# Performance work log

Hardware: AMD Instinct MI355X
Metric: run time of the kernel (lower is better)

Reference implementation:

```python
import jax, jax.numpy as jnp
import numpy as np
from jax import lax

H = 1024
VOCAB = 32000
B = 64
T = 256
PAD_IDX = 0


def setup_inputs() -> dict:
    key = jax.random.key(0)
    ks = jax.random.split(key, 10)
    tgt = jax.random.randint(ks[0], (B, T), 0, VOCAB, dtype=jnp.int64)
    h0 = jax.random.normal(ks[1], (1, B, H), dtype=jnp.float32)
    c0 = jax.random.normal(ks[2], (1, B, H), dtype=jnp.float32)
    encoder_outputs = jax.random.normal(ks[3], (B, 64, H), dtype=jnp.float32)
    src_lengths = jax.random.randint(ks[4], (B,), 1, 64, dtype=jnp.int64)
    # Embedding table; padding_idx row is zero (as nn.Embedding with padding_idx)
    scale = 1.0 / np.sqrt(H)
    emb = jax.random.normal(ks[5], (VOCAB, H), dtype=jnp.float32)
    emb = emb.at[PAD_IDX].set(0.0)
    # LSTM params, PyTorch layout: W_ih [4H, H], W_hh [4H, H], gate order i,f,g,o
    W_ih = jax.random.uniform(ks[6], (4 * H, H), minval=-scale, maxval=scale, dtype=jnp.float32)
    W_hh = jax.random.uniform(ks[7], (4 * H, H), minval=-scale, maxval=scale, dtype=jnp.float32)
    b_ih = jax.random.uniform(ks[8], (4 * H,), minval=-scale, maxval=scale, dtype=jnp.float32)
    b_hh = jax.random.uniform(ks[9], (4 * H,), minval=-scale, maxval=scale, dtype=jnp.float32)
    return {"tgt": tgt, "h0": h0, "c0": c0, "encoder_outputs": encoder_outputs,
            "src_lengths": src_lengths, "emb": emb,
            "W_ih": W_ih, "W_hh": W_hh, "b_ih": b_ih, "b_hh": b_hh}


def reference(tgt, h0, c0, encoder_outputs, src_lengths, emb, W_ih, W_hh, b_ih, b_hh):
    # Dropout in eval mode => identity. attn / encoder_outputs / src_lengths unused in math.
    x = emb[tgt]                      # [B, T, H] embedding lookup
    bias = b_ih + b_hh                # [4H]
    # Precompute input projections for all steps at once (same math, one big GEMM)
    x_proj = jnp.einsum('bth,gh->btg', x, W_ih) + bias   # [B, T, 4H]

    def step(carry, xp_t):
        h, c = carry                  # [B, H] each
        gates = xp_t + h @ W_hh.T     # [B, 4H]
        i, f, g, o = jnp.split(gates, 4, axis=-1)
        c_new = jax.nn.sigmoid(f) * c + jax.nn.sigmoid(i) * jnp.tanh(g)
        h_new = jax.nn.sigmoid(o) * jnp.tanh(c_new)
        return (h_new, c_new), h_new

    (h_fin, c_fin), ys = lax.scan(step, (h0[0], c0[0]),
                                  jnp.swapaxes(x_proj, 0, 1))   # scan over T
    outputs = jnp.swapaxes(ys, 0, 1)  # [B, T, H]
    return outputs, (h_fin[None], c_fin[None])
```

## Files before the change

### kernel.cpp

```cpp
#include <hip/hip_runtime.h>
#include <hip/hip_bf16.h>
#include <math.h>

#define B    64
#define T    256
#define H    1024
#define G4   4096
#define TC   64
#define NCH  (T / TC)
#define NBLK 128
#define FSTR 16

typedef __attribute__((ext_vector_type(8))) short bf16x8;
typedef __attribute__((ext_vector_type(4))) float f32x4;

__device__ __forceinline__ unsigned short f2bf(float x) {
    union { float f; unsigned u; } v; v.f = x;
    unsigned r = v.u + 0x7fffu + ((v.u >> 16) & 1u);
    return (unsigned short)(r >> 16);
}
__device__ __forceinline__ float bf2f(unsigned short s) {
    union { unsigned u; float f; } v; v.u = ((unsigned)s) << 16;
    return v.f;
}
__device__ __forceinline__ float sigm_f(float x) {
    return 1.f / (1.f + __expf(-x));
}
__device__ __forceinline__ float tanh_f(float x) {
    float e = __expf(2.f * x);
    return (e - 1.f) / (e + 1.f);
}

__global__ __launch_bounds__(256) void cast_f32_bf16(
    const float* __restrict__ src, unsigned short* __restrict__ dst, int n8)
{
    int i = blockIdx.x * 256 + threadIdx.x;
    if (i >= n8) return;
    const float4* s = (const float4*)(src + (size_t)i * 8);
    float4 a = s[0], b = s[1];
    bf16x8 o;
    o[0] = f2bf(a.x); o[1] = f2bf(a.y); o[2] = f2bf(a.z); o[3] = f2bf(a.w);
    o[4] = f2bf(b.x); o[5] = f2bf(b.y); o[6] = f2bf(b.z); o[7] = f2bf(b.w);
    *(bf16x8*)(dst + (size_t)i * 8) = o;
}

__global__ __launch_bounds__(256) void gather_x(
    const int* __restrict__ tgt, const float* __restrict__ emb,
    unsigned short* __restrict__ xch, int t0)
{
    int tid = threadIdx.x;
    int r   = blockIdx.x * 2 + (tid >> 7);
    int c   = (tid & 127) * 8;
    int b   = r & 63, tcc = r >> 6;
    int token = tgt[b * T + t0 + tcc];
    const float4* s = (const float4*)(emb + (size_t)token * H + c);
    float4 x0 = s[0], x1 = s[1];
    bf16x8 o;
    o[0] = f2bf(x0.x); o[1] = f2bf(x0.y); o[2] = f2bf(x0.z); o[3] = f2bf(x0.w);
    o[4] = f2bf(x1.x); o[5] = f2bf(x1.y); o[6] = f2bf(x1.z); o[7] = f2bf(x1.w);
    *(bf16x8*)(xch + (size_t)r * H + c) = o;
}

__global__ __launch_bounds__(256) void gemm_xproj(
    const unsigned short* __restrict__ A,
    const unsigned short* __restrict__ Bt,
    unsigned short* __restrict__ C)
{
    __shared__ unsigned short As[128 * 64], Bs[128 * 64];
    const int tid  = threadIdx.x;
    const int brow = (blockIdx.x >> 5) * 128;
    const int bcol = (blockIdx.x & 31) * 128;
    const int w = tid >> 6, lane = tid & 63;
    const int wr = w >> 1, wc = w & 1;
    const int lr = lane & 15, lg = lane >> 4;

    f32x4 acc[4][4] = {};

    for (int kc = 0; kc < H; kc += 64) {
        if (kc) __syncthreads();
        #pragma unroll
        for (int i = 0; i < 4; ++i) {
            int sf  = i * 256 + tid;
            int row = sf >> 3, s = sf & 7;
            int col = kc + s * 8;
            *(bf16x8*)(As + row * 64 + ((s ^ (row & 7)) * 8)) =
                *(const bf16x8*)(A + (size_t)(brow + row) * H + col);
            *(bf16x8*)(Bs + row * 64 + ((s ^ (row & 7)) * 8)) =
                *(const bf16x8*)(Bt + (size_t)(bcol + row) * H + col);
        }
        __syncthreads();
        #pragma unroll
        for (int kk = 0; kk < 2; ++kk) {
            bf16x8 af[4], bv[4];
            #pragma unroll
            for (int m = 0; m < 4; ++m) {
                int row = wr * 64 + m * 16 + lr;
                int s   = kk * 4 + lg;
                af[m] = *(const bf16x8*)(As + row * 64 + ((s ^ (row & 7)) * 8));
            }
            #pragma unroll
            for (int n = 0; n < 4; ++n) {
                int row = wc * 64 + n * 16 + lr;
                int s   = kk * 4 + lg;
                bv[n] = *(const bf16x8*)(Bs + row * 64 + ((s ^ (row & 7)) * 8));
            }
            #pragma unroll
            for (int m = 0; m < 4; ++m)
                #pragma unroll
                for (int n = 0; n < 4; ++n)
                    acc[m][n] = __builtin_amdgcn_mfma_f32_16x16x32_bf16(
                        af[m], bv[n], acc[m][n], 0, 0, 0);
        }
    }
    #pragma unroll
    for (int m = 0; m < 4; ++m)
        #pragma unroll
        for (int n = 0; n < 4; ++n)
            #pragma unroll
            for (int r = 0; r < 4; ++r) {
                int row = brow + wr * 64 + m * 16 + lg * 4 + r;
                int col = bcol + wc * 64 + n * 16 + lr;
                C[(size_t)row * G4 + col] = f2bf(acc[m][n][r]);
            }
}

__global__ __launch_bounds__(512) void lstm_chunk(
    const unsigned short* __restrict__ xproj,
    const unsigned short* __restrict__ whh,
    const float* __restrict__ bih, const float* __restrict__ bhh,
    unsigned short* __restrict__ hchain,
    float* __restrict__ cbuf,
    float* __restrict__ outputs,
    int* __restrict__ flags,
    int t0)
{
    __shared__ bf16x8 Ws[32 * 128];
    __shared__ float  gst[2][64][36];

    const int tid = threadIdx.x;
    const int jb  = blockIdx.x;
    const int j0  = jb * 8;

    #pragma unroll
    for (int it = 0; it < 8; ++it) {
        int f = it * 512 + tid;
        int v = f >> 7, s = f & 127;
        int grow = (v >> 3) * H + j0 + (v & 7);
        Ws[v * 128 + (s ^ (v & 7))] =
            *(const bf16x8*)(whh + (size_t)grow * H + s * 8);
    }

    const int w = tid >> 6, lane = tid & 63;
    const int m = w & 3, kh = w >> 2;
    const int lr = lane & 15, lg = lane >> 4;
    const int vx = lr & 7;

    const int b_e  = tid >> 3;
    const int jc_e = tid & 7;
    const int hj   = j0 + jc_e;
    float breg[4];
    #pragma unroll
    for (int qq = 0; qq < 4; ++qq)
        breg[qq] = bih[qq * H + hj] + bhh[qq * H + hj];
    float creg = cbuf[b_e * H + hj];
    __syncthreads();

    for (int tc8 = 0; tc8 < TC; tc8 += 8) {
        float oreg[8];
        #pragma unroll
        for (int p = 0; p < 8; ++p) {
            const int tcs    = tc8 + p;
            const int target = t0 + tcs;

            float xpv[4];
            #pragma unroll
            for (int qq = 0; qq < 4; ++qq)
                xpv[qq] = bf2f(xproj[((size_t)tcs * B + b_e) * G4
                                     + qq * H + hj]);

            const unsigned short* hc     = hchain + (size_t)tcs * B * H;
            unsigned short*       hn_buf = hchain + (size_t)(tcs + 1) * B * H;

            while (true) {
                int fv = __hip_atomic_load(&flags[(kh * 64 + lane) * FSTR],
                            __ATOMIC_RELAXED, __HIP_MEMORY_SCOPE_AGENT);
                if (__all(fv >= target)) break;
                __builtin_amdgcn_s_sleep(1);
            }

            __builtin_amdgcn_s_setprio(1);
            f32x4 acc0 = {}, acc1 = {};
            #pragma unroll
            for (int ks = 0; ks < 16; ++ks) {
                int s = kh * 64 + ks * 4 + lg;
                bf16x8 av = *(const bf16x8*)(hc
                    + ((size_t)s * 64 + m * 16 + lr) * 8);
                bf16x8 bw0 = Ws[lr * 128 + (s ^ vx)];
                bf16x8 bw1 = Ws[(16 + lr) * 128 + (s ^ vx)];
                acc0 = __builtin_amdgcn_mfma_f32_16x16x32_bf16(av, bw0, acc0,
                                                               0, 0, 0);
                acc1 = __builtin_amdgcn_mfma_f32_16x16x32_bf16(av, bw1, acc1,
                                                               0, 0, 0);
            }
            __builtin_amdgcn_s_setprio(0);
            #pragma unroll
            for (int r = 0; r < 4; ++r) {
                gst[kh][m * 16 + lg * 4 + r][lr]      = acc0[r];
                gst[kh][m * 16 + lg * 4 + r][16 + lr] = acc1[r];
            }
            __syncthreads();

            {
                float g[4];
                #pragma unroll
                for (int qq = 0; qq < 4; ++qq)
                    g[qq] = gst[0][b_e][qq * 8 + jc_e]
                          + gst[1][b_e][qq * 8 + jc_e]
                          + breg[qq] + xpv[qq];
                float ig = sigm_f(g[0]);
                float fg = sigm_f(g[1]);
                float gg = tanh_f(g[2]);
                float og = sigm_f(g[3]);
                float cn = fg * creg + ig * gg;
                float hnv = og * tanh_f(cn);
                creg = cn;
                oreg[p] = hnv;
                unsigned my = (unsigned)f2bf(hnv);
                unsigned ot = __shfl_xor(my, 1);
                if ((lane & 1) == 0) {
                    unsigned u = my | (ot << 16);
                    unsigned* dst = (unsigned*)(hn_buf
                        + (size_t)(jb * 64 + b_e) * 8 + jc_e);
                    __hip_atomic_store(dst, u, __ATOMIC_RELAXED,
                                       __HIP_MEMORY_SCOPE_AGENT);
                }
            }
            __syncthreads();

            if (tid == 0)
                __hip_atomic_store(&flags[jb * FSTR], target + 1,
                                   __ATOMIC_RELAXED, __HIP_MEMORY_SCOPE_AGENT);
        }
        #pragma unroll
        for (int p = 0; p < 8; ++p) {
            int t = t0 + tc8 + p;
            outputs[((size_t)b_e * T + t) * H + hj] = oreg[p];
        }
    }

    cbuf[b_e * H + hj] = creg;
}

__global__ __launch_bounds__(256) void init_state(
    const float* __restrict__ h0, const float* __restrict__ c0,
    unsigned short* __restrict__ hb, float* __restrict__ cb)
{
    int i = blockIdx.x * 256 + threadIdx.x;
    int b = i >> 10, j = i & 1023;
    hb[(size_t)(j >> 3) * 512 + b * 8 + (j & 7)] = f2bf(h0[i]);
    cb[i] = c0[i];
}

__global__ __launch_bounds__(128) void reset_flags(int* __restrict__ flags)
{
    __hip_atomic_store(&flags[threadIdx.x * FSTR], 0,
                       __ATOMIC_RELAXED, __HIP_MEMORY_SCOPE_AGENT);
}

__global__ __launch_bounds__(256) void copy_h(
    const unsigned short* __restrict__ src, unsigned short* __restrict__ dst)
{
    int i = blockIdx.x * 256 + threadIdx.x;
    ((unsigned*)dst)[i] = ((const unsigned*)src)[i];
}

__global__ __launch_bounds__(256) void finalize(
    const float* __restrict__ outputs, const float* __restrict__ cfin,
    float* __restrict__ outh, float* __restrict__ outc)
{
    int i = blockIdx.x * 256 + threadIdx.x;
    int b = i >> 10, j = i & 1023;
    outh[i] = outputs[((size_t)b * T + (T - 1)) * H + j];
    outc[i] = cfin[i];
}

extern "C" void kernel_launch(void* const* d_in, const int* in_sizes, int n_in,
                              void* d_out, int out_size, void* d_ws, size_t ws_size,
                              hipStream_t stream)
{
    const int*   tgt = (const int*)  d_in[0];
    const float* h0  = (const float*)d_in[1];
    const float* c0  = (const float*)d_in[2];
    const float* emb = (const float*)d_in[5];
    const float* Wih = (const float*)d_in[6];
    const float* Whh = (const float*)d_in[7];
    const float* bih = (const float*)d_in[8];
    const float* bhh = (const float*)d_in[9];

    float* out     = (float*)d_out;
    float* outputs = out;
    float* out_h   = out + (size_t)B * T * H;
    float* out_c   = out_h + B * H;

    unsigned short* xproj  = (unsigned short*)d_ws;
    unsigned short* xch    = xproj  + (size_t)TC * B * G4;
    unsigned short* wih    = xch    + (size_t)TC * B * H;
    unsigned short* whh    = wih    + (size_t)G4 * H;
    unsigned short* hchain = whh    + (size_t)G4 * H;
    float*          cbuf   = (float*)(hchain + (size_t)(TC + 1) * B * H);
    int*            flags  = (int*)(cbuf + (size_t)B * H);

    cast_f32_bf16<<<2048, 256, 0, stream>>>(Wih, wih, (G4 * H) / 8);
    cast_f32_bf16<<<2048, 256, 0, stream>>>(Whh, whh, (G4 * H) / 8);
    init_state<<<(B * H) / 256, 256, 0, stream>>>(h0, c0, hchain, cbuf);
    reset_flags<<<1, NBLK, 0, stream>>>(flags);

    for (int ci = 0; ci < NCH; ++ci) {
        gather_x<<<(TC * B) / 2, 256, 0, stream>>>(tgt, emb, xch, ci * TC);
        gemm_xproj<<<(TC * B / 128) * (G4 / 128), 256, 0, stream>>>(xch, wih, xproj);
        if (ci) copy_h<<<(B * H / 2) / 256, 256, 0, stream>>>(
                    hchain + (size_t)TC * B * H, hchain);
        int t0 = ci * TC;
        void* args[] = { (void*)&xproj, (void*)&whh, (void*)&bih, (void*)&bhh,
                         (void*)&hchain, (void*)&cbuf, (void*)&outputs,
                         (void*)&flags, (void*)&t0 };
        hipLaunchCooperativeKernel((void*)lstm_chunk, dim3(NBLK), dim3(512),
                                   args, 0, stream);
    }
    finalize<<<(B * H) / 256, 256, 0, stream>>>(outputs, cbuf, out_h, out_c);
}
```

Measured before the change: 1.286 ms.

## Replace block barriers with per-wave flags and full-K MFMA per wave

Each wave now covers the whole K dimension for its own 8 batch rows, so the shared-memory partial-sum reduction and both __syncthreads per timestep go away. Gate values are redistributed with lane shuffles, and every wave publishes its own progress flag (1024 flags instead of 128). The per-step wait polls only the producer waves that hold the h rows this wave reads. This shortens the cross-block dependency chain on each timestep, at the cost of twice the MFMA work per wave (half of each tile wasted on duplicated rows) and more flag polling traffic.

```diff
diff --git a/kernel.cpp b/kernel.cpp
--- a/kernel.cpp
+++ b/kernel.cpp
@@ -135,7 +135,6 @@
     int t0)
 {
     __shared__ bf16x8 Ws[32 * 128];
-    __shared__ float  gst[2][64][36];
 
     const int tid = threadIdx.x;
     const int jb  = blockIdx.x;
@@ -151,13 +150,17 @@
     }
 
     const int w = tid >> 6, lane = tid & 63;
-    const int m = w & 3, kh = w >> 2;
-    const int lr = lane & 15, lg = lane >> 4;
-    const int vx = lr & 7;
-
-    const int b_e  = tid >> 3;
-    const int jc_e = tid & 7;
+    const int lr  = lane & 15, lg = lane >> 4;
+    const int la7 = lane & 7;
+    const int vx  = lr & 7;
+
+    const int b_e  = w * 8 + (lane >> 3);
+    const int jc_e = lane & 7;
     const int hj   = j0 + jc_e;
+    const int rsel = (lane >> 3) & 3;
+    const int src0 = ((lane >> 5) << 4) + la7;
+    const int src1 = src0 + 8;
+
     float breg[4];
     #pragma unroll
     for (int qq = 0; qq < 4; ++qq)
@@ -182,19 +185,24 @@
             unsigned short*       hn_buf = hchain + (size_t)(tcs + 1) * B * H;
 
             while (true) {
-                int fv = __hip_atomic_load(&flags[(kh * 64 + lane) * FSTR],
-                            __ATOMIC_RELAXED, __HIP_MEMORY_SCOPE_AGENT);
-                if (__all(fv >= target)) break;
+                int f1 = __hip_atomic_load(
+                    &flags[(lane * 8 + w) * FSTR],
+                    __ATOMIC_RELAXED, __HIP_MEMORY_SCOPE_AGENT);
+                int f2 = __hip_atomic_load(
+                    &flags[((64 + lane) * 8 + w) * FSTR],
+                    __ATOMIC_RELAXED, __HIP_MEMORY_SCOPE_AGENT);
+                if (__all(f1 >= target && f2 >= target)) break;
                 __builtin_amdgcn_s_sleep(1);
             }
+            asm volatile("" ::: "memory");
 
             __builtin_amdgcn_s_setprio(1);
             f32x4 acc0 = {}, acc1 = {};
             #pragma unroll
-            for (int ks = 0; ks < 16; ++ks) {
-                int s = kh * 64 + ks * 4 + lg;
+            for (int ks = 0; ks < 32; ++ks) {
+                int s = ks * 4 + lg;
                 bf16x8 av = *(const bf16x8*)(hc
-                    + ((size_t)s * 64 + m * 16 + lr) * 8);
+                    + ((size_t)s * 64 + w * 8 + la7) * 8);
                 bf16x8 bw0 = Ws[lr * 128 + (s ^ vx)];
                 bf16x8 bw1 = Ws[(16 + lr) * 128 + (s ^ vx)];
                 acc0 = __builtin_amdgcn_mfma_f32_16x16x32_bf16(av, bw0, acc0,
@@ -203,24 +211,26 @@
                                                                0, 0, 0);
             }
             __builtin_amdgcn_s_setprio(0);
+
+            float g0 = 0.f, g1 = 0.f, g2 = 0.f, g3 = 0.f;
             #pragma unroll
             for (int r = 0; r < 4; ++r) {
-                gst[kh][m * 16 + lg * 4 + r][lr]      = acc0[r];
-                gst[kh][m * 16 + lg * 4 + r][16 + lr] = acc1[r];
-            }
-            __syncthreads();
+                float v00 = __shfl(acc0[r], src0);
+                float v01 = __shfl(acc0[r], src1);
+                float v10 = __shfl(acc1[r], src0);
+                float v11 = __shfl(acc1[r], src1);
+                if (rsel == r) { g0 = v00; g1 = v01; g2 = v10; g3 = v11; }
+            }
 
             {
-                float g[4];
-                #pragma unroll
-                for (int qq = 0; qq < 4; ++qq)
-                    g[qq] = gst[0][b_e][qq * 8 + jc_e]
-                          + gst[1][b_e][qq * 8 + jc_e]
-                          + breg[qq] + xpv[qq];
-                float ig = sigm_f(g[0]);
-                float fg = sigm_f(g[1]);
-                float gg = tanh_f(g[2]);
-                float og = sigm_f(g[3]);
+                g0 += breg[0] + xpv[0];
+                g1 += breg[1] + xpv[1];
+                g2 += breg[2] + xpv[2];
+                g3 += breg[3] + xpv[3];
+                float ig = sigm_f(g0);
+                float fg = sigm_f(g1);
+                float gg = tanh_f(g2);
+                float og = sigm_f(g3);
                 float cn = fg * creg + ig * gg;
                 float hnv = og * tanh_f(cn);
                 creg = cn;
@@ -235,10 +245,9 @@
                                        __HIP_MEMORY_SCOPE_AGENT);
                 }
             }
-            __syncthreads();
-
-            if (tid == 0)
-                __hip_atomic_store(&flags[jb * FSTR], target + 1,
+            asm volatile("s_waitcnt vmcnt(0)" ::: "memory");
+            if (lane == 0)
+                __hip_atomic_store(&flags[(jb * 8 + w) * FSTR], target + 1,
                                    __ATOMIC_RELAXED, __HIP_MEMORY_SCOPE_AGENT);
         }
         #pragma unroll
@@ -261,9 +270,10 @@
     cb[i] = c0[i];
 }
 
-__global__ __launch_bounds__(128) void reset_flags(int* __restrict__ flags)
-{
-    __hip_atomic_store(&flags[threadIdx.x * FSTR], 0,
+__global__ __launch_bounds__(256) void reset_flags(int* __restrict__ flags)
+{
+    int i = blockIdx.x * 256 + threadIdx.x;
+    __hip_atomic_store(&flags[i * FSTR], 0,
                        __ATOMIC_RELAXED, __HIP_MEMORY_SCOPE_AGENT);
 }
 
@@ -313,7 +323,7 @@
     cast_f32_bf16<<<2048, 256, 0, stream>>>(Wih, wih, (G4 * H) / 8);
     cast_f32_bf16<<<2048, 256, 0, stream>>>(Whh, whh, (G4 * H) / 8);
     init_state<<<(B * H) / 256, 256, 0, stream>>>(h0, c0, hchain, cbuf);
-    reset_flags<<<1, NBLK, 0, stream>>>(flags);
+    reset_flags<<<4, 256, 0, stream>>>(flags);
 
     for (int ci = 0; ci < NCH; ++ci) {
         gather_x<<<(TC * B) / 2, 256, 0, stream>>>(tgt, emb, xch, ci * TC);
```

After: 3.454 ms. +168.5%, slower.

## Overlap next-chunk input projection GEMM with recurrent LSTM chunk in one kernel

Applied to the files above, without the earlier changes.

Merges the embedding gather into the input-projection GEMM by reading embedding rows and converting them to bf16 while filling shared memory. The cooperative kernel now launches twice as many blocks: the extra blocks compute the next chunk's input projections into a double buffer while the first 128 blocks run the serial recurrence. The hidden-state chain becomes a ring buffer, which removes the copy_h kernel. Chunk size drops to 32 timesteps. The aim is to hide the GEMM and extra launches behind the latency-bound recurrence. The risk is that the GEMM blocks compete for CUs and memory bandwidth with the recurrent blocks on the critical path, and that twice as many chunk launches are needed.

```diff
diff --git a/kernel.cpp b/kernel.cpp
--- a/kernel.cpp
+++ b/kernel.cpp
@@ -6,9 +6,10 @@
 #define T    256
 #define H    1024
 #define G4   4096
-#define TC   64
+#define TC   32
 #define NCH  (T / TC)
 #define NBLK 128
+#define NSLOT (TC + 1)
 #define FSTR 16
 
 typedef __attribute__((ext_vector_type(8))) short bf16x8;
@@ -44,47 +45,42 @@
     *(bf16x8*)(dst + (size_t)i * 8) = o;
 }
 
-__global__ __launch_bounds__(256) void gather_x(
+__device__ __forceinline__ void xproj_tile(
     const int* __restrict__ tgt, const float* __restrict__ emb,
-    unsigned short* __restrict__ xch, int t0)
-{
-    int tid = threadIdx.x;
-    int r   = blockIdx.x * 2 + (tid >> 7);
-    int c   = (tid & 127) * 8;
-    int b   = r & 63, tcc = r >> 6;
-    int token = tgt[b * T + t0 + tcc];
-    const float4* s = (const float4*)(emb + (size_t)token * H + c);
-    float4 x0 = s[0], x1 = s[1];
-    bf16x8 o;
-    o[0] = f2bf(x0.x); o[1] = f2bf(x0.y); o[2] = f2bf(x0.z); o[3] = f2bf(x0.w);
-    o[4] = f2bf(x1.x); o[5] = f2bf(x1.y); o[6] = f2bf(x1.z); o[7] = f2bf(x1.w);
-    *(bf16x8*)(xch + (size_t)r * H + c) = o;
-}
-
-__global__ __launch_bounds__(256) void gemm_xproj(
-    const unsigned short* __restrict__ A,
-    const unsigned short* __restrict__ Bt,
-    unsigned short* __restrict__ C)
-{
-    __shared__ unsigned short As[128 * 64], Bs[128 * 64];
-    const int tid  = threadIdx.x;
-    const int brow = (blockIdx.x >> 5) * 128;
-    const int bcol = (blockIdx.x & 31) * 128;
-    const int w = tid >> 6, lane = tid & 63;
+    const unsigned short* __restrict__ Bt, unsigned short* __restrict__ C,
+    int t0, int brow, int bcol,
+    unsigned short* AsB, int* toks, int t256)
+{
+    unsigned short* As = AsB;
+    unsigned short* Bs = AsB + 128 * 64;
+    const int w = t256 >> 6, lane = t256 & 63;
     const int wr = w >> 1, wc = w & 1;
     const int lr = lane & 15, lg = lane >> 4;
 
+    if (t256 < 128) {
+        int r = brow + t256;
+        toks[t256] = tgt[(r & 63) * T + t0 + (r >> 6)];
+    }
+    __syncthreads();
+
     f32x4 acc[4][4] = {};
 
     for (int kc = 0; kc < H; kc += 64) {
         if (kc) __syncthreads();
         #pragma unroll
         for (int i = 0; i < 4; ++i) {
-            int sf  = i * 256 + tid;
+            int sf  = i * 256 + t256;
             int row = sf >> 3, s = sf & 7;
             int col = kc + s * 8;
-            *(bf16x8*)(As + row * 64 + ((s ^ (row & 7)) * 8)) =
-                *(const bf16x8*)(A + (size_t)(brow + row) * H + col);
+            const float4* sa = (const float4*)(emb
+                + (size_t)toks[row] * H + col);
+            float4 a0 = sa[0], a1 = sa[1];
+            bf16x8 av;
+            av[0] = f2bf(a0.x); av[1] = f2bf(a0.y);
+            av[2] = f2bf(a0.z); av[3] = f2bf(a0.w);
+            av[4] = f2bf(a1.x); av[5] = f2bf(a1.y);
+            av[6] = f2bf(a1.z); av[7] = f2bf(a1.w);
+            *(bf16x8*)(As + row * 64 + ((s ^ (row & 7)) * 8)) = av;
             *(bf16x8*)(Bs + row * 64 + ((s ^ (row & 7)) * 8)) =
                 *(const bf16x8*)(Bt + (size_t)(bcol + row) * H + col);
         }
@@ -122,9 +118,23 @@
                 int col = bcol + wc * 64 + n * 16 + lr;
                 C[(size_t)row * G4 + col] = f2bf(acc[m][n][r]);
             }
-}
-
-__global__ __launch_bounds__(512) void lstm_chunk(
+    __syncthreads();
+}
+
+__global__ __launch_bounds__(256) void gemm_xproj(
+    const int* __restrict__ tgt, const float* __restrict__ emb,
+    const unsigned short* __restrict__ wih, unsigned short* __restrict__ xp,
+    int t0)
+{
+    __shared__ __align__(16) unsigned char smem[33280];
+    unsigned short* AsB = (unsigned short*)smem;
+    int* toks = (int*)(smem + 32768);
+    int tile = blockIdx.x;
+    xproj_tile(tgt, emb, wih, xp, t0,
+               (tile >> 5) * 128, (tile & 31) * 128, AsB, toks, threadIdx.x);
+}
+
+__global__ __launch_bounds__(512) void lstm_fused(
     const unsigned short* __restrict__ xproj,
     const unsigned short* __restrict__ whh,
     const float* __restrict__ bih, const float* __restrict__ bhh,
@@ -132,14 +142,38 @@
     float* __restrict__ cbuf,
     float* __restrict__ outputs,
     int* __restrict__ flags,
-    int t0)
-{
-    __shared__ bf16x8 Ws[32 * 128];
-    __shared__ float  gst[2][64][36];
-
+    int t0,
+    const int* __restrict__ tgt, const float* __restrict__ emb,
+    const unsigned short* __restrict__ wih,
+    unsigned short* __restrict__ xpn,
+    int t0n, int do_gemm)
+{
+    __shared__ __align__(16) unsigned char smem[83968];
     const int tid = threadIdx.x;
-    const int jb  = blockIdx.x;
-    const int j0  = jb * 8;
+    const int bid = blockIdx.x;
+
+    if (bid >= NBLK) {
+        if (!do_gemm) return;
+        const int sub  = tid >> 8;
+        const int t256 = tid & 255;
+        unsigned char* base = smem + sub * 33280;
+        unsigned short* AsB = (unsigned short*)base;
+        int* toks = (int*)(base + 32768);
+        const int gb = bid - NBLK;
+        #pragma unroll
+        for (int i = 0; i < 2; ++i) {
+            int tile = i * 256 + gb * 2 + sub;
+            xproj_tile(tgt, emb, wih, xpn, t0n,
+                       (tile >> 5) * 128, (tile & 31) * 128, AsB, toks, t256);
+        }
+        return;
+    }
+
+    bf16x8* Ws = (bf16x8*)smem;
+    float (*gst)[64][36] = (float (*)[64][36])(smem + 65536);
+
+    const int jb = bid;
+    const int j0 = jb * 8;
 
     #pragma unroll
     for (int it = 0; it < 8; ++it) {
@@ -165,6 +199,8 @@
     float creg = cbuf[b_e * H + hj];
     __syncthreads();
 
+    int sl = t0 % NSLOT;
+
     for (int tc8 = 0; tc8 < TC; tc8 += 8) {
         float oreg[8];
         #pragma unroll
@@ -178,8 +214,9 @@
                 xpv[qq] = bf2f(xproj[((size_t)tcs * B + b_e) * G4
                                      + qq * H + hj]);
 
-            const unsigned short* hc     = hchain + (size_t)tcs * B * H;
-            unsigned short*       hn_buf = hchain + (size_t)(tcs + 1) * B * H;
+            const unsigned short* hc = hchain + (size_t)sl * (B * H);
+            const int sln = (sl + 1 == NSLOT) ? 0 : sl + 1;
+            unsigned short* hn_buf = hchain + (size_t)sln * (B * H);
 
             while (true) {
                 int fv = __hip_atomic_load(&flags[(kh * 64 + lane) * FSTR],
@@ -240,6 +277,7 @@
             if (tid == 0)
                 __hip_atomic_store(&flags[jb * FSTR], target + 1,
                                    __ATOMIC_RELAXED, __HIP_MEMORY_SCOPE_AGENT);
+            sl = sln;
         }
         #pragma unroll
         for (int p = 0; p < 8; ++p) {
@@ -265,13 +303,6 @@
 {
     __hip_atomic_store(&flags[threadIdx.x * FSTR], 0,
                        __ATOMIC_RELAXED, __HIP_MEMORY_SCOPE_AGENT);
-}
-
-__global__ __launch_bounds__(256) void copy_h(
-    const unsigned short* __restrict__ src, unsigned short* __restrict__ dst)
-{
-    int i = blockIdx.x * 256 + threadIdx.x;
-    ((unsigned*)dst)[i] = ((const unsigned*)src)[i];
 }
 
 __global__ __launch_bounds__(256) void finalize(
@@ -302,30 +333,36 @@
     float* out_h   = out + (size_t)B * T * H;
     float* out_c   = out_h + B * H;
 
-    unsigned short* xproj  = (unsigned short*)d_ws;
-    unsigned short* xch    = xproj  + (size_t)TC * B * G4;
-    unsigned short* wih    = xch    + (size_t)TC * B * H;
-    unsigned short* whh    = wih    + (size_t)G4 * H;
-    unsigned short* hchain = whh    + (size_t)G4 * H;
-    float*          cbuf   = (float*)(hchain + (size_t)(TC + 1) * B * H);
+    unsigned short* xp0    = (unsigned short*)d_ws;
+    unsigned short* xp1    = xp0 + (size_t)TC * B * G4;
+    unsigned short* wih    = xp1 + (size_t)TC * B * G4;
+    unsigned short* whh    = wih + (size_t)G4 * H;
+    unsigned short* hchain = whh + (size_t)G4 * H;
+    float*          cbuf   = (float*)(hchain + (size_t)NSLOT * B * H);
     int*            flags  = (int*)(cbuf + (size_t)B * H);
+    unsigned short* xp[2]  = { xp0, xp1 };
 
     cast_f32_bf16<<<2048, 256, 0, stream>>>(Wih, wih, (G4 * H) / 8);
     cast_f32_bf16<<<2048, 256, 0, stream>>>(Whh, whh, (G4 * H) / 8);
     init_state<<<(B * H) / 256, 256, 0, stream>>>(h0, c0, hchain, cbuf);
     reset_flags<<<1, NBLK, 0, stream>>>(flags);
 
+    gemm_xproj<<<(TC * B / 128) * (G4 / 128), 256, 0, stream>>>(
+        tgt, emb, wih, xp[0], 0);
+
     for (int ci = 0; ci < NCH; ++ci) {
-        gather_x<<<(TC * B) / 2, 256, 0, stream>>>(tgt, emb, xch, ci * TC);
-        gemm_xproj<<<(TC * B / 128) * (G4 / 128), 256, 0, stream>>>(xch, wih, xproj);
-        if (ci) copy_h<<<(B * H / 2) / 256, 256, 0, stream>>>(
-                    hchain + (size_t)TC * B * H, hchain);
-        int t0 = ci * TC;
-        void* args[] = { (void*)&xproj, (void*)&whh, (void*)&bih, (void*)&bhh,
+        int t0  = ci * TC;
+        int t0n = (ci + 1) * TC;
+        int dg  = (ci + 1 < NCH) ? 1 : 0;
+        const unsigned short* xc = xp[ci & 1];
+        unsigned short*       xn = xp[(ci + 1) & 1];
+        void* args[] = { (void*)&xc, (void*)&whh, (void*)&bih, (void*)&bhh,
                          (void*)&hchain, (void*)&cbuf, (void*)&outputs,
-                         (void*)&flags, (void*)&t0 };
-        hipLaunchCooperativeKernel((void*)lstm_chunk, dim3(NBLK), dim3(512),
-                                   args, 0, stream);
+                         (void*)&flags, (void*)&t0,
+                         (void*)&tgt, (void*)&emb, (void*)&wih,
+                         (void*)&xn, (void*)&t0n, (void*)&dg };
+        hipLaunchCooperativeKernel((void*)lstm_fused, dim3(2 * NBLK),
+                                   dim3(512), args, 0, stream);
     }
     finalize<<<(B * H) / 256, 256, 0, stream>>>(outputs, cbuf, out_h, out_c);
 }
```

Result: faster. 1.232 ms, median of 2 (-4.2%).
